# Performance work log

Measured on AMD Instinct MI355X. Metric: run time of the kernel, lower is better.

## Reference

```python
import jax, jax.numpy as jnp
import numpy as np

B = 2
C = 96
NH = 4
HD = C // NH
DEPTH = 2
LAT, LON = 181, 360
WH, WW = 6, 12
N = WH * WW
PT, PBm, PL, PR = 2, 3, 0, 0
H, W = LAT + PT + PBm, LON + PL + PR
SH, SW = WH // 2, WW // 2
NWH, NWW = H // WH, W // WW
NW = NWH * NWW
SCALE = HD ** -0.5

def _rel_index():
    ch, cw = np.meshgrid(np.arange(WH), np.arange(WW), indexing='ij')
    coords = np.stack([ch, cw]).reshape(2, -1)
    rel = (coords[:, :, None] - coords[:, None, :]).transpose(1, 2, 0).astype(np.int64)
    rel[:, :, 0] += WH - 1
    rel[:, :, 1] += WW - 1
    rel[:, :, 0] *= 2 * WW - 1
    return rel.sum(-1)  # (N, N)

REL_IDX = jnp.asarray(_rel_index())

def _shift_mask():
    img = np.zeros((H, W))
    cnt = 0
    for hs in (slice(0, -WH), slice(-WH, -SH), slice(-SH, None)):
        for ws in (slice(0, -WW), slice(-WW, -SW), slice(-SW, None)):
            img[hs, ws] = cnt
            cnt += 1
    mw = img.reshape(NWH, WH, NWW, WW).transpose(0, 2, 1, 3).reshape(NW, N)
    am = mw[:, None, :] - mw[:, :, None]
    return np.where(am != 0, -100.0, 0.0).astype(np.float32)

ATTN_MASK = jnp.asarray(_shift_mask())  # (NW, N, N)

def _ln(x, g, b):
    m = x.mean(-1, keepdims=True)
    v = x.var(-1, keepdims=True)
    return (x - m) * jax.lax.rsqrt(v + 1e-5) * g + b

def _win_part(x):
    b = x.shape[0]
    return x.reshape(b, NWH, WH, NWW, WW, C).transpose(0, 1, 3, 2, 4, 5).reshape(-1, N, C)

def _win_rev(xw, b):
    return xw.reshape(b, NWH, NWW, WH, WW, C).transpose(0, 1, 3, 2, 4, 5).reshape(b, H, W, C)

def _block(x, shift, g1, b1, qw, qb, pw, pb, rpb, g2, b2, f1w, f1b, f2w, f2b):
    b = x.shape[0]
    sc = x
    x = _ln(x, g1, b1)
    if shift:
        x = jnp.roll(x, (-SH, -SW), (1, 2))
    xw = _win_part(x)  # (b*NW, N, C)
    qkv = (xw @ qw.T + qb).reshape(-1, N, 3, NH, HD).transpose(2, 0, 3, 1, 4)
    q, k, v = qkv[0], qkv[1], qkv[2]  # each (b*NW, NH, N, HD)
    attn = (q * SCALE) @ k.transpose(0, 1, 3, 2)  # (b*NW, NH, N, N)
    bias = rpb[REL_IDX].transpose(2, 0, 1)  # (NH, N, N)
    attn = attn + bias[None]
    if shift:
        attn = (attn.reshape(b, NW, NH, N, N) + ATTN_MASK[None, :, None]).reshape(-1, NH, N, N)
    attn = jax.nn.softmax(attn, axis=-1)
    out = (attn @ v).transpose(0, 2, 1, 3).reshape(-1, N, C)
    out = out @ pw.T + pb
    x = _win_rev(out, b)
    if shift:
        x = jnp.roll(x, (SH, SW), (1, 2))
    x = sc + x
    h = _ln(x, g2, b2)
    h = jax.nn.gelu(h @ f1w.T + f1b) @ f2w.T + f2b
    return x + h

def _forward(x, g1, b1, qkv_w, qkv_b, proj_w, proj_b, rpb, g2, b2, fc1_w, fc1_b, fc2_w, fc2_b):
    x = jnp.pad(x, ((0, 0), (0, 0), (PT, PBm), (PL, PR)))  # ZeroPad2d
    x = x.transpose(0, 2, 3, 1)  # (B, H, W, C)
    for i in range(DEPTH):
        x = _block(x, i % 2 == 1, g1[i], b1[i], qkv_w[i], qkv_b[i], proj_w[i], proj_b[i],
                   rpb[i], g2[i], b2[i], fc1_w[i], fc1_b[i], fc2_w[i], fc2_b[i])
    x = x.transpose(0, 3, 1, 2)
    return x[:, :, PT:H - PBm, PL:W - PR]


def setup_inputs() -> dict:
    key = jax.random.key(0)
    ks = jax.random.split(key, 6)
    s = 0.02
    tbl = (2 * WH - 1) * (2 * WW - 1)
    return {
        'x': jax.random.normal(ks[0], (B, C, LAT, LON), jnp.float32),
        'g1': jnp.ones((DEPTH, C), jnp.float32),
        'b1': jnp.zeros((DEPTH, C), jnp.float32),
        'qkv_w': jax.random.normal(ks[1], (DEPTH, 3 * C, C), jnp.float32) * s,
        'qkv_b': jnp.zeros((DEPTH, 3 * C), jnp.float32),
        'proj_w': jax.random.normal(ks[2], (DEPTH, C, C), jnp.float32) * s,
        'proj_b': jnp.zeros((DEPTH, C), jnp.float32),
        'rpb': jax.random.normal(ks[3], (DEPTH, tbl, NH), jnp.float32) * s,
        'g2': jnp.ones((DEPTH, C), jnp.float32),
        'b2': jnp.zeros((DEPTH, C), jnp.float32),
        'fc1_w': jax.random.normal(ks[4], (DEPTH, 4 * C, C), jnp.float32) * s,
        'fc1_b': jnp.zeros((DEPTH, 4 * C), jnp.float32),
        'fc2_w': jax.random.normal(ks[5], (DEPTH, C, 4 * C), jnp.float32) * s,
        'fc2_b': jnp.zeros((DEPTH, C), jnp.float32),
    }


def reference(x, g1, b1, qkv_w, qkv_b, proj_w, proj_b, rpb, g2, b2, fc1_w, fc1_b, fc2_w, fc2_b):
    return _forward(x, g1, b1, qkv_w, qkv_b, proj_w, proj_b, rpb, g2, b2, fc1_w, fc1_b, fc2_w, fc2_b)
```

## Files before the change

kernel.cpp:

```cpp
#include <hip/hip_runtime.h>
#include <hip/hip_bf16.h>
#include <math.h>

#define BB    2
#define CC    96
#define NHD   4
#define HDIM  24
#define LAT_  181
#define LON_  360
#define PT_   2
#define HH    186
#define WWID  360
#define WH_   6
#define WW_   12
#define NTOK  72
#define SH_   3
#define SW_   6
#define NWH_  31
#define NWW_  30
#define NWIN  930
#define SCALE_ 0.20412414523193154f

typedef __attribute__((ext_vector_type(8))) short short8v;
typedef __attribute__((ext_vector_type(4))) float f32x4;

__device__ __forceinline__ unsigned short pk_bf16(float x) {
    __hip_bfloat16 h = __float2bfloat16(x);
    union { __hip_bfloat16 b; unsigned short u; } cv; cv.b = h; return cv.u;
}
__device__ __forceinline__ uint2 pk4(float a, float b, float c, float d) {
    __hip_bfloat162 lo = __float22bfloat162_rn(make_float2(a, b));
    __hip_bfloat162 hi = __float22bfloat162_rn(make_float2(c, d));
    union { __hip_bfloat162 b; unsigned u; } c0, c1; c0.b = lo; c1.b = hi;
    uint2 r; r.x = c0.u; r.y = c1.u; return r;
}

__global__ __launch_bounds__(256) void k_pad2(const float* __restrict__ in, float* __restrict__ X) {
    int bid = blockIdx.x;
    int ct = bid % 3; bid /= 3;
    int wt = bid % 12; bid /= 12;
    int h = bid % HH; int b = bid / HH;
    int lat = h - PT_;
    int tx = threadIdx.x & 31, ty = threadIdx.x >> 5;
    __shared__ float tile[32][33];
    if (lat >= 0 && lat < LAT_) {
        int w = wt * 32 + tx;
        #pragma unroll
        for (int i = 0; i < 4; ++i) {
            int c = ct * 32 + ty + 8 * i;
            float v = 0.f;
            if (w < WWID) v = in[((long)(b * CC + c)) * (LAT_ * LON_) + lat * LON_ + w];
            tile[ty + 8 * i][tx] = v;
        }
    } else {
        #pragma unroll
        for (int i = 0; i < 4; ++i) tile[ty + 8 * i][tx] = 0.f;
    }
    __syncthreads();
    #pragma unroll
    for (int i = 0; i < 4; ++i) {
        int w = wt * 32 + ty + 8 * i;
        if (w < WWID)
            X[(((long)(b * HH + h)) * WWID + w) * CC + ct * 32 + tx] = tile[tx][ty + 8 * i];
    }
}

__global__ __launch_bounds__(256) void k_crop2(const float* __restrict__ X, float* __restrict__ out) {
    int bid = blockIdx.x;
    int ct = bid % 3; bid /= 3;
    int wt = bid % 12; bid /= 12;
    int lat = bid % LAT_; int b = bid / LAT_;
    int h = lat + PT_;
    int tx = threadIdx.x & 31, ty = threadIdx.x >> 5;
    __shared__ float tile[32][33];
    #pragma unroll
    for (int i = 0; i < 4; ++i) {
        int w = wt * 32 + ty + 8 * i;
        if (w < WWID)
            tile[ty + 8 * i][tx] = X[(((long)(b * HH + h)) * WWID + w) * CC + ct * 32 + tx];
    }
    __syncthreads();
    {
        int w = wt * 32 + tx;
        if (w < WWID) {
            #pragma unroll
            for (int i = 0; i < 4; ++i) {
                int c = ct * 32 + ty + 8 * i;
                out[((long)(b * CC + c)) * (LAT_ * LON_) + lat * LON_ + w] = tile[tx][ty + 8 * i];
            }
        }
    }
}

__global__ void k_wprep(const float* __restrict__ f1w, const float* __restrict__ f2w,
                        const float* __restrict__ qkvw, const float* __restrict__ projw,
                        const float* __restrict__ rpb,
                        unsigned short* __restrict__ wbf, float* __restrict__ biasg) {
    int id = blockIdx.x * 256 + threadIdx.x;
    if (id < 73728) {
        int layer = id / 36864, rem = id % 36864;
        int ks = rem / 12288, r2 = rem % 12288;
        int nt = r2 / 512, r3 = r2 % 512;
        int lane = r3 / 8, e = r3 % 8;
        int o = nt * 16 + (lane & 15);
        int c = ks * 32 + 8 * (lane >> 4) + e;
        wbf[(long)layer * 36864 + rem] = pk_bf16(f1w[((long)layer * 384 + o) * 96 + c]);
    } else if (id < 147456) {
        int id2 = id - 73728;
        int layer = id2 / 36864, rem = id2 % 36864;
        int ks = rem / 3072, r2 = rem % 3072;
        int nt = r2 / 512, r3 = r2 % 512;
        int lane = r3 / 8, e = r3 % 8;
        int o = nt * 16 + (lane & 15);
        int c = ks * 32 + 8 * (lane >> 4) + e;
        wbf[73728 + (long)layer * 36864 + rem] = pk_bf16(f2w[((long)layer * 96 + o) * 384 + c]);
    } else if (id < 202752) {
        wbf[id] = pk_bf16(qkvw[id - 147456]);
    } else if (id < 221184) {
        wbf[id] = pk_bf16(projw[id - 202752]);
    } else {
        int id2 = id - 221184;
        int layer = id2 / 102400, r = id2 % 102400;
        int type = r / 25600; r %= 25600;
        int h = r / 6400; r %= 6400;
        int i = r / 80, j = r % 80;
        float v;
        if (i >= 72 || j >= 72) {
            v = -10000.f;
        } else {
            int thi = i / 12, twi = i % 12, thj = j / 12, twj = j % 12;
            int ridx = (thi - thj + 5) * 23 + (twi - twj + 11);
            v = rpb[(layer * 253 + ridx) * 4 + h];
            if (layer == 1) {
                int eh = type & 1, ew = type >> 1;
                int ri = (eh ? (thi < 3 ? 1 : 2) * 3 : 0) + (ew ? (twi < 6 ? 1 : 2) : 0);
                int rj = (eh ? (thj < 3 ? 1 : 2) * 3 : 0) + (ew ? (twj < 6 ? 1 : 2) : 0);
                if (ri != rj) v -= 100.f;
            }
        }
        biasg[id2] = v;
    }
}

template <int SHIFT>
__global__ __launch_bounds__(1024, 4) void k_attn(float* __restrict__ X,
        const float* __restrict__ gg, const float* __restrict__ bb,
        const unsigned short* __restrict__ wqkv, const float* __restrict__ qkvb,
        const unsigned short* __restrict__ wprj, const float* __restrict__ projb,
        const float* __restrict__ biasT) {
    __shared__ __align__(16) unsigned char smem[127232];
    unsigned short* As  = (unsigned short*)smem;
    unsigned short* psw0= (unsigned short*)smem;
    unsigned short* qs  = (unsigned short*)(smem + 53248);
    unsigned short* ks  = (unsigned short*)(smem + 68608);
    unsigned short* vt  = (unsigned short*)(smem + 83968);
    unsigned short* os  = (unsigned short*)(smem + 110592);

    int bid = blockIdx.x;
    int b = bid / NWIN, wi = bid % NWIN;
    int nwh = wi / NWW_, nww = wi % NWW_;
    int tid = threadIdx.x;
    int wv = tid >> 6, lane = tid & 63;
    int li = lane & 15, gq = lane >> 4;

    int type = SHIFT ? ((nwh == 30 ? 1 : 0) | (nww == 29 ? 2 : 0)) : 0;
    const float* bias_t = biasT + type * 25600;

    {
        unsigned* vz = (unsigned*)vt;
        for (int idx = tid; idx < 6656; idx += 1024) vz[idx] = 0u;
        unsigned* az = (unsigned*)(As + 72 * 104);
        for (int idx = tid; idx < 416; idx += 1024) az[idx] = 0u;
    }

    {
        int sub = lane >> 3, p = lane & 7;
        int t = wv * 8 + sub;
        if (t < 72) {
            int th = t / 12, tw = t % 12;
            int hr = nwh * WH_ + th, wr = nww * WW_ + tw;
            int ho = SHIFT ? (hr + SH_) % HH : hr;
            int wo = SHIFT ? (wr + SW_) % WWID : wr;
            const float* xr = X + (((long)b * HH + ho) * WWID + wo) * CC;
            float4 a  = *(const float4*)(xr + p * 4);
            float4 c4 = *(const float4*)(xr + p * 4 + 32);
            float4 e4 = *(const float4*)(xr + p * 4 + 64);
            float s  = a.x + a.y + a.z + a.w + c4.x + c4.y + c4.z + c4.w + e4.x + e4.y + e4.z + e4.w;
            float sq = a.x*a.x + a.y*a.y + a.z*a.z + a.w*a.w + c4.x*c4.x + c4.y*c4.y + c4.z*c4.z + c4.w*c4.w
                     + e4.x*e4.x + e4.y*e4.y + e4.z*e4.z + e4.w*e4.w;
            #pragma unroll
            for (int off = 1; off < 8; off <<= 1) {
                s  += __shfl_xor(s, off);
                sq += __shfl_xor(sq, off);
            }
            float mean = s * (1.f / CC);
            float var = sq * (1.f / CC) - mean * mean;
            float rs = rsqrtf(var + 1e-5f);
            float4 g0 = *(const float4*)(gg + p * 4);
            float4 g1v = *(const float4*)(gg + p * 4 + 32);
            float4 g2v = *(const float4*)(gg + p * 4 + 64);
            float4 t0 = *(const float4*)(bb + p * 4);
            float4 t1 = *(const float4*)(bb + p * 4 + 32);
            float4 t2 = *(const float4*)(bb + p * 4 + 64);
            *(uint2*)(As + t * 104 + p * 4) =
                pk4((a.x - mean) * rs * g0.x + t0.x, (a.y - mean) * rs * g0.y + t0.y,
                    (a.z - mean) * rs * g0.z + t0.z, (a.w - mean) * rs * g0.w + t0.w);
            *(uint2*)(As + t * 104 + p * 4 + 32) =
                pk4((c4.x - mean) * rs * g1v.x + t1.x, (c4.y - mean) * rs * g1v.y + t1.y,
                    (c4.z - mean) * rs * g1v.z + t1.z, (c4.w - mean) * rs * g1v.w + t1.w);
            *(uint2*)(As + t * 104 + p * 4 + 64) =
                pk4((e4.x - mean) * rs * g2v.x + t2.x, (e4.y - mean) * rs * g2v.y + t2.y,
                    (e4.z - mean) * rs * g2v.z + t2.z, (e4.w - mean) * rs * g2v.w + t2.w);
        }
    }
    __syncthreads();

    for (int mt = wv; mt < 18; mt += 16) {
        short8v aw[3];
        #pragma unroll
        for (int ksi = 0; ksi < 3; ++ksi)
            aw[ksi] = *(const short8v*)(wqkv + (mt * 16 + li) * 96 + ksi * 32 + 8 * gq);
        float bias4[4];
        #pragma unroll
        for (int r = 0; r < 4; ++r) bias4[r] = qkvb[mt * 16 + 4 * gq + r];
        f32x4 acc[5];
        #pragma unroll
        for (int nt = 0; nt < 5; ++nt) acc[nt] = (f32x4){0.f, 0.f, 0.f, 0.f};
        #pragma unroll
        for (int nt = 0; nt < 5; ++nt)
            #pragma unroll
            for (int ksi = 0; ksi < 3; ++ksi) {
                short8v by = *(const short8v*)(As + (nt * 16 + li) * 104 + ksi * 32 + 8 * gq);
                acc[nt] = __builtin_amdgcn_mfma_f32_16x16x32_bf16(aw[ksi], by, acc[nt], 0, 0, 0);
            }
        int which = mt / 6, mtl = mt % 6;
        int oo0 = mtl * 16 + 4 * gq;
        int h = oo0 / 24, d0 = oo0 % 24;
        #pragma unroll
        for (int nt = 0; nt < 5; ++nt) {
            int token = nt * 16 + li;
            if (which == 2) {
                #pragma unroll
                for (int r = 0; r < 4; ++r)
                    vt[(h * 32 + d0 + r) * 104 + token] = pk_bf16(acc[nt][r] + bias4[r]);
            } else {
                float v0 = acc[nt][0] + bias4[0], v1 = acc[nt][1] + bias4[1];
                float v2 = acc[nt][2] + bias4[2], v3 = acc[nt][3] + bias4[3];
                if (which == 0) { v0 *= SCALE_; v1 *= SCALE_; v2 *= SCALE_; v3 *= SCALE_; }
                unsigned short* dst = (which == 0 ? qs : ks) + (h * 80 + token) * 24 + d0;
                *(uint2*)dst = pk4(v0, v1, v2, v3);
            }
        }
    }
    __syncthreads();

    for (int u = wv; u < 20; u += 16) {
        int h = u / 5, nt = u % 5;
        unsigned short* psw = psw0 + (size_t)wv * (16 * 104);
        *(uint2*)(psw + li * 104 + 80 + 4 * gq) = (uint2){0u, 0u};
        short8v bq = {0,0,0,0,0,0,0,0};
        if (gq < 3) bq = *(const short8v*)(qs + (h * 80 + nt * 16 + li) * 24 + 8 * gq);
        const float* brow = bias_t + (h * 80 + nt * 16 + li) * 80;
        float p[20];
        float sum = 0.f;
        #pragma unroll
        for (int mt = 0; mt < 5; ++mt) {
            short8v ak = {0,0,0,0,0,0,0,0};
            if (gq < 3) ak = *(const short8v*)(ks + (h * 80 + mt * 16 + li) * 24 + 8 * gq);
            f32x4 ct = __builtin_amdgcn_mfma_f32_16x16x32_bf16(ak, bq, (f32x4){0.f,0.f,0.f,0.f}, 0, 0, 0);
            float4 bv = *(const float4*)(brow + mt * 16 + 4 * gq);
            p[mt*4+0] = __expf(ct[0] + bv.x);
            p[mt*4+1] = __expf(ct[1] + bv.y);
            p[mt*4+2] = __expf(ct[2] + bv.z);
            p[mt*4+3] = __expf(ct[3] + bv.w);
            sum += p[mt*4+0] + p[mt*4+1] + p[mt*4+2] + p[mt*4+3];
        }
        sum += __shfl_xor(sum, 16);
        sum += __shfl_xor(sum, 32);
        float inv = sum > 0.f ? 1.f / sum : 0.f;
        #pragma unroll
        for (int mt = 0; mt < 5; ++mt)
            *(uint2*)(psw + li * 104 + mt * 16 + 4 * gq) =
                pk4(p[mt*4+0] * inv, p[mt*4+1] * inv, p[mt*4+2] * inv, p[mt*4+3] * inv);
        #pragma unroll
        for (int nt2 = 0; nt2 < 2; ++nt2) {
            f32x4 acc = (f32x4){0.f, 0.f, 0.f, 0.f};
            #pragma unroll
            for (int ksi = 0; ksi < 3; ++ksi) {
                short8v ap = *(const short8v*)(psw + li * 104 + ksi * 32 + 8 * gq);
                short8v bv = *(const short8v*)(vt + (h * 32 + nt2 * 16 + li) * 104 + ksi * 32 + 8 * gq);
                acc = __builtin_amdgcn_mfma_f32_16x16x32_bf16(ap, bv, acc, 0, 0, 0);
            }
            int d = nt2 * 16 + li;
            if (d < 24) {
                #pragma unroll
                for (int r = 0; r < 4; ++r)
                    os[(nt * 16 + 4 * gq + r) * 104 + h * 24 + d] = pk_bf16(acc[r]);
            }
        }
    }
    __syncthreads();

    for (int u = wv; u < 30; u += 16) {
        int mt = u / 6, nt = u % 6;
        f32x4 acc = (f32x4){0.f, 0.f, 0.f, 0.f};
        #pragma unroll
        for (int ksi = 0; ksi < 3; ++ksi) {
            short8v ao = *(const short8v*)(os + (mt * 16 + li) * 104 + ksi * 32 + 8 * gq);
            short8v bw = *(const short8v*)(wprj + (nt * 16 + li) * 96 + ksi * 32 + 8 * gq);
            acc = __builtin_amdgcn_mfma_f32_16x16x32_bf16(ao, bw, acc, 0, 0, 0);
        }
        int o = nt * 16 + li;
        float bo = projb[o];
        #pragma unroll
        for (int r = 0; r < 4; ++r) {
            int token = mt * 16 + 4 * gq + r;
            if (token < 72) {
                int th = token / 12, tw = token % 12;
                int hr = nwh * WH_ + th, wr = nww * WW_ + tw;
                int ho = SHIFT ? (hr + SH_) % HH : hr;
                int wo = SHIFT ? (wr + SW_) % WWID : wr;
                X[(((long)b * HH + ho) * WWID + wo) * CC + o] += acc[r] + bo;
            }
        }
    }
}

__global__ __launch_bounds__(256, 4) void k_mlp_mfma(float* __restrict__ X,
        const float* __restrict__ g, const float* __restrict__ bta,
        const unsigned short* __restrict__ w1f, const float* __restrict__ b1v,
        const unsigned short* __restrict__ w2f, const float* __restrict__ b2v) {
    __shared__ __align__(16) unsigned short As[32 * 120];
    __shared__ __align__(16) unsigned short Hs[32 * 392];
    long tok0 = (long)blockIdx.x * 32;
    int tid = threadIdx.x;

    {
        int t = tid >> 3, p = tid & 7;
        const float* xr = X + (tok0 + t) * CC;
        float4 a = *(const float4*)(xr + p * 4);
        float4 b = *(const float4*)(xr + p * 4 + 32);
        float4 c4 = *(const float4*)(xr + p * 4 + 64);
        float s  = a.x + a.y + a.z + a.w + b.x + b.y + b.z + b.w + c4.x + c4.y + c4.z + c4.w;
        float sq = a.x*a.x + a.y*a.y + a.z*a.z + a.w*a.w + b.x*b.x + b.y*b.y + b.z*b.z + b.w*b.w
                 + c4.x*c4.x + c4.y*c4.y + c4.z*c4.z + c4.w*c4.w;
        #pragma unroll
        for (int off = 1; off < 8; off <<= 1) {
            s  += __shfl_xor(s, off);
            sq += __shfl_xor(sq, off);
        }
        float mean = s * (1.f / CC);
        float var = sq * (1.f / CC) - mean * mean;
        float rs = rsqrtf(var + 1e-5f);
        float4 g0 = *(const float4*)(g + p * 4);
        float4 g1 = *(const float4*)(g + p * 4 + 32);
        float4 g2 = *(const float4*)(g + p * 4 + 64);
        float4 t0 = *(const float4*)(bta + p * 4);
        float4 t1 = *(const float4*)(bta + p * 4 + 32);
        float4 t2 = *(const float4*)(bta + p * 4 + 64);
        unsigned short* arow = As + t * 120;
        *(uint2*)(arow + p * 4) =
            pk4((a.x - mean) * rs * g0.x + t0.x, (a.y - mean) * rs * g0.y + t0.y,
                (a.z - mean) * rs * g0.z + t0.z, (a.w - mean) * rs * g0.w + t0.w);
        *(uint2*)(arow + p * 4 + 32) =
            pk4((b.x - mean) * rs * g1.x + t1.x, (b.y - mean) * rs * g1.y + t1.y,
                (b.z - mean) * rs * g1.z + t1.z, (b.w - mean) * rs * g1.w + t1.w);
        *(uint2*)(arow + p * 4 + 64) =
            pk4((c4.x - mean) * rs * g2.x + t2.x, (c4.y - mean) * rs * g2.y + t2.y,
                (c4.z - mean) * rs * g2.z + t2.z, (c4.w - mean) * rs * g2.w + t2.w);
    }
    __syncthreads();

    int w = tid >> 6, lane = tid & 63;
    int wm = w & 1;
    int row = wm * 16 + (lane & 15);
    int kbase = 8 * (lane >> 4);

    {
        int wnh = w >> 1;
        short8v afr[3];
        #pragma unroll
        for (int ks = 0; ks < 3; ++ks)
            afr[ks] = *(const short8v*)(As + row * 120 + ks * 32 + kbase);
        f32x4 acc[12];
        #pragma unroll
        for (int j = 0; j < 12; ++j) acc[j] = (f32x4){0.f, 0.f, 0.f, 0.f};
        const short8v* wb = (const short8v*)w1f;
        #pragma unroll
        for (int j = 0; j < 12; ++j) {
            int nt = wnh * 12 + j;
            #pragma unroll
            for (int ks = 0; ks < 3; ++ks) {
                short8v bfr = wb[(ks * 24 + nt) * 64 + lane];
                acc[j] = __builtin_amdgcn_mfma_f32_16x16x32_bf16(afr[ks], bfr, acc[j], 0, 0, 0);
            }
        }
        #pragma unroll
        for (int j = 0; j < 12; ++j) {
            int n = (wnh * 12 + j) * 16 + (lane & 15);
            float bb = b1v[n];
            #pragma unroll
            for (int r = 0; r < 4; ++r) {
                float s = acc[j][r] + bb;
                float z = s + 0.044715f * s * s * s;
                float gl = s / (1.f + __expf(-1.5957691216057308f * z));
                Hs[(wm * 16 + 4 * (lane >> 4) + r) * 392 + n] = pk_bf16(gl);
            }
        }
    }
    __syncthreads();

    {
        int wnt0 = (w >> 1) * 3;
        f32x4 acc2[3];
        #pragma unroll
        for (int j = 0; j < 3; ++j) acc2[j] = (f32x4){0.f, 0.f, 0.f, 0.f};
        const short8v* wb2 = (const short8v*)w2f;
        #pragma unroll
        for (int ks = 0; ks < 12; ++ks) {
            short8v a2 = *(const short8v*)(Hs + row * 392 + ks * 32 + kbase);
            #pragma unroll
            for (int j = 0; j < 3; ++j) {
                short8v bfr = wb2[(ks * 6 + wnt0 + j) * 64 + lane];
                acc2[j] = __builtin_amdgcn_mfma_f32_16x16x32_bf16(a2, bfr, acc2[j], 0, 0, 0);
            }
        }
        #pragma unroll
        for (int j = 0; j < 3; ++j) {
            int n = (wnt0 + j) * 16 + (lane & 15);
            float bb = b2v[n];
            #pragma unroll
            for (int r = 0; r < 4; ++r) {
                long tok = tok0 + wm * 16 + 4 * (lane >> 4) + r;
                X[tok * CC + n] += acc2[j][r] + bb;
            }
        }
    }
}

extern "C" void kernel_launch(void* const* d_in, const int* in_sizes, int n_in,
                              void* d_out, int out_size, void* d_ws, size_t ws_size,
                              hipStream_t stream) {
    const float* x     = (const float*)d_in[0];
    const float* g1    = (const float*)d_in[1];
    const float* b1    = (const float*)d_in[2];
    const float* qkvw  = (const float*)d_in[3];
    const float* qkvb  = (const float*)d_in[4];
    const float* projw = (const float*)d_in[5];
    const float* projb = (const float*)d_in[6];
    const float* rpb   = (const float*)d_in[7];
    const float* g2    = (const float*)d_in[8];
    const float* b2    = (const float*)d_in[9];
    const float* f1w   = (const float*)d_in[10];
    const float* f1b   = (const float*)d_in[11];
    const float* f2w   = (const float*)d_in[12];
    const float* f2b   = (const float*)d_in[13];

    float* X = (float*)d_ws;
    unsigned short* wbf = (unsigned short*)(X + (long)BB * HH * WWID * CC);
    float* biasg = (float*)(wbf + 221184);

    const int ntok = BB * HH * WWID;

    k_pad2<<<BB * HH * 12 * 3, 256, 0, stream>>>(x, X);
    k_wprep<<<1664, 256, 0, stream>>>(f1w, f2w, qkvw, projw, rpb, wbf, biasg);

    for (int i = 0; i < 2; ++i) {
        const unsigned short* wqkv_bf = wbf + 147456 + (long)i * 27648;
        const unsigned short* wprj_bf = wbf + 202752 + (long)i * 9216;
        if (i == 0) {
            k_attn<0><<<BB * NWIN, 1024, 0, stream>>>(X, g1, b1,
                wqkv_bf, qkvb, wprj_bf, projb, biasg);
        } else {
            k_attn<1><<<BB * NWIN, 1024, 0, stream>>>(X, g1 + CC, b1 + CC,
                wqkv_bf, qkvb + 3 * CC, wprj_bf, projb + CC, biasg + 102400);
        }
        k_mlp_mfma<<<ntok / 32, 256, 0, stream>>>(X,
            g2 + i * CC, b2 + i * CC,
            wbf + (long)i * 36864, f1b + i * 4 * CC,
            wbf + 73728 + (long)i * 36864, f2b + i * CC);
    }

    k_crop2<<<BB * LAT_ * 12 * 3, 256, 0, stream>>>(X, (float*)d_out);
}
```

Baseline: 326.7 us.

## Fuse MLP block into windowed attention kernel per window

The second LayerNorm and the two-layer MLP now run inside the attention kernel. The post-projection residual is kept in shared memory (Xn) for the window's 72 tokens, so the separate MLP kernel launch and a full read-modify-write pass over X in global memory go away. The cost is that the MLP now runs in 1024-thread blocks with heavy shared memory use, which limits occupancy. It also wastes work on padded rows, since 80 rows are computed for 72 tokens.

```diff
diff --git a/kernel.cpp b/kernel.cpp
--- a/kernel.cpp
+++ b/kernel.cpp
@@ -147,7 +147,10 @@
         const float* __restrict__ gg, const float* __restrict__ bb,
         const unsigned short* __restrict__ wqkv, const float* __restrict__ qkvb,
         const unsigned short* __restrict__ wprj, const float* __restrict__ projb,
-        const float* __restrict__ biasT) {
+        const float* __restrict__ biasT,
+        const float* __restrict__ g2, const float* __restrict__ b2,
+        const unsigned short* __restrict__ w1f, const float* __restrict__ b1v,
+        const unsigned short* __restrict__ w2f, const float* __restrict__ b2v) {
     __shared__ __align__(16) unsigned char smem[127232];
     unsigned short* As  = (unsigned short*)smem;
     unsigned short* psw0= (unsigned short*)smem;
@@ -155,6 +158,9 @@
     unsigned short* ks  = (unsigned short*)(smem + 68608);
     unsigned short* vt  = (unsigned short*)(smem + 83968);
     unsigned short* os  = (unsigned short*)(smem + 110592);
+    float* Xn           = (float*)smem;
+    unsigned short* A2s = (unsigned short*)(smem + 33280);
+    unsigned short* Hs  = (unsigned short*)(smem + 53248);
 
     int bid = blockIdx.x;
     int b = bid / NWIN, wi = bid % NWIN;
@@ -172,7 +178,6 @@
         unsigned* az = (unsigned*)(As + 72 * 104);
         for (int idx = tid; idx < 416; idx += 1024) az[idx] = 0u;
     }
-
     {
         int sub = lane >> 3, p = lane & 7;
         int t = wv * 8 + sub;
@@ -320,119 +325,102 @@
                 int hr = nwh * WH_ + th, wr = nww * WW_ + tw;
                 int ho = SHIFT ? (hr + SH_) % HH : hr;
                 int wo = SHIFT ? (wr + SW_) % WWID : wr;
-                X[(((long)b * HH + ho) * WWID + wo) * CC + o] += acc[r] + bo;
-            }
-        }
-    }
-}
-
-__global__ __launch_bounds__(256, 4) void k_mlp_mfma(float* __restrict__ X,
-        const float* __restrict__ g, const float* __restrict__ bta,
-        const unsigned short* __restrict__ w1f, const float* __restrict__ b1v,
-        const unsigned short* __restrict__ w2f, const float* __restrict__ b2v) {
-    __shared__ __align__(16) unsigned short As[32 * 120];
-    __shared__ __align__(16) unsigned short Hs[32 * 392];
-    long tok0 = (long)blockIdx.x * 32;
-    int tid = threadIdx.x;
+                float xo = X[(((long)b * HH + ho) * WWID + wo) * CC + o];
+                Xn[token * 104 + o] = xo + acc[r] + bo;
+            }
+        }
+    }
+    __syncthreads();
 
     {
-        int t = tid >> 3, p = tid & 7;
-        const float* xr = X + (tok0 + t) * CC;
-        float4 a = *(const float4*)(xr + p * 4);
-        float4 b = *(const float4*)(xr + p * 4 + 32);
-        float4 c4 = *(const float4*)(xr + p * 4 + 64);
-        float s  = a.x + a.y + a.z + a.w + b.x + b.y + b.z + b.w + c4.x + c4.y + c4.z + c4.w;
-        float sq = a.x*a.x + a.y*a.y + a.z*a.z + a.w*a.w + b.x*b.x + b.y*b.y + b.z*b.z + b.w*b.w
-                 + c4.x*c4.x + c4.y*c4.y + c4.z*c4.z + c4.w*c4.w;
-        #pragma unroll
-        for (int off = 1; off < 8; off <<= 1) {
-            s  += __shfl_xor(s, off);
-            sq += __shfl_xor(sq, off);
-        }
-        float mean = s * (1.f / CC);
-        float var = sq * (1.f / CC) - mean * mean;
-        float rs = rsqrtf(var + 1e-5f);
-        float4 g0 = *(const float4*)(g + p * 4);
-        float4 g1 = *(const float4*)(g + p * 4 + 32);
-        float4 g2 = *(const float4*)(g + p * 4 + 64);
-        float4 t0 = *(const float4*)(bta + p * 4);
-        float4 t1 = *(const float4*)(bta + p * 4 + 32);
-        float4 t2 = *(const float4*)(bta + p * 4 + 64);
-        unsigned short* arow = As + t * 120;
-        *(uint2*)(arow + p * 4) =
-            pk4((a.x - mean) * rs * g0.x + t0.x, (a.y - mean) * rs * g0.y + t0.y,
-                (a.z - mean) * rs * g0.z + t0.z, (a.w - mean) * rs * g0.w + t0.w);
-        *(uint2*)(arow + p * 4 + 32) =
-            pk4((b.x - mean) * rs * g1.x + t1.x, (b.y - mean) * rs * g1.y + t1.y,
-                (b.z - mean) * rs * g1.z + t1.z, (b.w - mean) * rs * g1.w + t1.w);
-        *(uint2*)(arow + p * 4 + 64) =
-            pk4((c4.x - mean) * rs * g2.x + t2.x, (c4.y - mean) * rs * g2.y + t2.y,
-                (c4.z - mean) * rs * g2.z + t2.z, (c4.w - mean) * rs * g2.w + t2.w);
-    }
-    __syncthreads();
-
-    int w = tid >> 6, lane = tid & 63;
-    int wm = w & 1;
-    int row = wm * 16 + (lane & 15);
-    int kbase = 8 * (lane >> 4);
-
+        unsigned* az = (unsigned*)(A2s + 72 * 104);
+        for (int idx = tid; idx < 416; idx += 1024) az[idx] = 0u;
+    }
     {
-        int wnh = w >> 1;
+        int sub = lane >> 3, p = lane & 7;
+        int t = wv * 8 + sub;
+        if (t < 72) {
+            const float* xr = Xn + t * 104;
+            float4 a  = *(const float4*)(xr + p * 4);
+            float4 c4 = *(const float4*)(xr + p * 4 + 32);
+            float4 e4 = *(const float4*)(xr + p * 4 + 64);
+            float s  = a.x + a.y + a.z + a.w + c4.x + c4.y + c4.z + c4.w + e4.x + e4.y + e4.z + e4.w;
+            float sq = a.x*a.x + a.y*a.y + a.z*a.z + a.w*a.w + c4.x*c4.x + c4.y*c4.y + c4.z*c4.z + c4.w*c4.w
+                     + e4.x*e4.x + e4.y*e4.y + e4.z*e4.z + e4.w*e4.w;
+            #pragma unroll
+            for (int off = 1; off < 8; off <<= 1) {
+                s  += __shfl_xor(s, off);
+                sq += __shfl_xor(sq, off);
+            }
+            float mean = s * (1.f / CC);
+            float var = sq * (1.f / CC) - mean * mean;
+            float rs = rsqrtf(var + 1e-5f);
+            float4 g0 = *(const float4*)(g2 + p * 4);
+            float4 g1v = *(const float4*)(g2 + p * 4 + 32);
+            float4 g2v = *(const float4*)(g2 + p * 4 + 64);
+            float4 t0 = *(const float4*)(b2 + p * 4);
+            float4 t1 = *(const float4*)(b2 + p * 4 + 32);
+            float4 t2 = *(const float4*)(b2 + p * 4 + 64);
+            *(uint2*)(A2s + t * 104 + p * 4) =
+                pk4((a.x - mean) * rs * g0.x + t0.x, (a.y - mean) * rs * g0.y + t0.y,
+                    (a.z - mean) * rs * g0.z + t0.z, (a.w - mean) * rs * g0.w + t0.w);
+            *(uint2*)(A2s + t * 104 + p * 4 + 32) =
+                pk4((c4.x - mean) * rs * g1v.x + t1.x, (c4.y - mean) * rs * g1v.y + t1.y,
+                    (c4.z - mean) * rs * g1v.z + t1.z, (c4.w - mean) * rs * g1v.w + t1.w);
+            *(uint2*)(A2s + t * 104 + p * 4 + 64) =
+                pk4((e4.x - mean) * rs * g2v.x + t2.x, (e4.y - mean) * rs * g2v.y + t2.y,
+                    (e4.z - mean) * rs * g2v.z + t2.z, (e4.w - mean) * rs * g2v.w + t2.w);
+        }
+    }
+    __syncthreads();
+
+    for (int u = wv; u < 120; u += 16) {
+        int mt = u / 24, nt = u % 24;
         short8v afr[3];
         #pragma unroll
-        for (int ks = 0; ks < 3; ++ks)
-            afr[ks] = *(const short8v*)(As + row * 120 + ks * 32 + kbase);
-        f32x4 acc[12];
-        #pragma unroll
-        for (int j = 0; j < 12; ++j) acc[j] = (f32x4){0.f, 0.f, 0.f, 0.f};
+        for (int ksi = 0; ksi < 3; ++ksi)
+            afr[ksi] = *(const short8v*)(A2s + (mt * 16 + li) * 104 + ksi * 32 + 8 * gq);
+        f32x4 acc = (f32x4){0.f, 0.f, 0.f, 0.f};
         const short8v* wb = (const short8v*)w1f;
         #pragma unroll
-        for (int j = 0; j < 12; ++j) {
-            int nt = wnh * 12 + j;
-            #pragma unroll
-            for (int ks = 0; ks < 3; ++ks) {
-                short8v bfr = wb[(ks * 24 + nt) * 64 + lane];
-                acc[j] = __builtin_amdgcn_mfma_f32_16x16x32_bf16(afr[ks], bfr, acc[j], 0, 0, 0);
-            }
-        }
-        #pragma unroll
-        for (int j = 0; j < 12; ++j) {
-            int n = (wnh * 12 + j) * 16 + (lane & 15);
-            float bb = b1v[n];
-            #pragma unroll
-            for (int r = 0; r < 4; ++r) {
-                float s = acc[j][r] + bb;
-                float z = s + 0.044715f * s * s * s;
-                float gl = s / (1.f + __expf(-1.5957691216057308f * z));
-                Hs[(wm * 16 + 4 * (lane >> 4) + r) * 392 + n] = pk_bf16(gl);
-            }
-        }
-    }
-    __syncthreads();
-
-    {
-        int wnt0 = (w >> 1) * 3;
-        f32x4 acc2[3];
-        #pragma unroll
-        for (int j = 0; j < 3; ++j) acc2[j] = (f32x4){0.f, 0.f, 0.f, 0.f};
+        for (int ksi = 0; ksi < 3; ++ksi) {
+            short8v bfr = wb[(ksi * 24 + nt) * 64 + lane];
+            acc = __builtin_amdgcn_mfma_f32_16x16x32_bf16(afr[ksi], bfr, acc, 0, 0, 0);
+        }
+        int n = nt * 16 + li;
+        float bb1 = b1v[n];
+        #pragma unroll
+        for (int r = 0; r < 4; ++r) {
+            float s = acc[r] + bb1;
+            float z = s + 0.044715f * s * s * s;
+            float gl = s / (1.f + __expf(-1.5957691216057308f * z));
+            Hs[(mt * 16 + 4 * gq + r) * 392 + n] = pk_bf16(gl);
+        }
+    }
+    __syncthreads();
+
+    for (int u = wv; u < 30; u += 16) {
+        int mt = u / 6, nt = u % 6;
+        f32x4 acc = (f32x4){0.f, 0.f, 0.f, 0.f};
         const short8v* wb2 = (const short8v*)w2f;
         #pragma unroll
-        for (int ks = 0; ks < 12; ++ks) {
-            short8v a2 = *(const short8v*)(Hs + row * 392 + ks * 32 + kbase);
-            #pragma unroll
-            for (int j = 0; j < 3; ++j) {
-                short8v bfr = wb2[(ks * 6 + wnt0 + j) * 64 + lane];
-                acc2[j] = __builtin_amdgcn_mfma_f32_16x16x32_bf16(a2, bfr, acc2[j], 0, 0, 0);
-            }
-        }
-        #pragma unroll
-        for (int j = 0; j < 3; ++j) {
-            int n = (wnt0 + j) * 16 + (lane & 15);
-            float bb = b2v[n];
-            #pragma unroll
-            for (int r = 0; r < 4; ++r) {
-                long tok = tok0 + wm * 16 + 4 * (lane >> 4) + r;
-                X[tok * CC + n] += acc2[j][r] + bb;
+        for (int ksi = 0; ksi < 12; ++ksi) {
+            short8v a2 = *(const short8v*)(Hs + (mt * 16 + li) * 392 + ksi * 32 + 8 * gq);
+            short8v bfr = wb2[(ksi * 6 + nt) * 64 + lane];
+            acc = __builtin_amdgcn_mfma_f32_16x16x32_bf16(a2, bfr, acc, 0, 0, 0);
+        }
+        int n = nt * 16 + li;
+        float bb2 = b2v[n];
+        #pragma unroll
+        for (int r = 0; r < 4; ++r) {
+            int token = mt * 16 + 4 * gq + r;
+            if (token < 72) {
+                int th = token / 12, tw = token % 12;
+                int hr = nwh * WH_ + th, wr = nww * WW_ + tw;
+                int ho = SHIFT ? (hr + SH_) % HH : hr;
+                int wo = SHIFT ? (wr + SW_) % WWID : wr;
+                X[(((long)b * HH + ho) * WWID + wo) * CC + n] =
+                    Xn[token * 104 + n] + acc[r] + bb2;
             }
         }
     }
@@ -460,25 +448,23 @@
     unsigned short* wbf = (unsigned short*)(X + (long)BB * HH * WWID * CC);
     float* biasg = (float*)(wbf + 221184);
 
-    const int ntok = BB * HH * WWID;
-
     k_pad2<<<BB * HH * 12 * 3, 256, 0, stream>>>(x, X);
     k_wprep<<<1664, 256, 0, stream>>>(f1w, f2w, qkvw, projw, rpb, wbf, biasg);
 
     for (int i = 0; i < 2; ++i) {
         const unsigned short* wqkv_bf = wbf + 147456 + (long)i * 27648;
         const unsigned short* wprj_bf = wbf + 202752 + (long)i * 9216;
+        const unsigned short* w1f = wbf + (long)i * 36864;
+        const unsigned short* w2f = wbf + 73728 + (long)i * 36864;
         if (i == 0) {
             k_attn<0><<<BB * NWIN, 1024, 0, stream>>>(X, g1, b1,
-                wqkv_bf, qkvb, wprj_bf, projb, biasg);
+                wqkv_bf, qkvb, wprj_bf, projb, biasg,
+                g2, b2, w1f, f1b, w2f, f2b);
         } else {
             k_attn<1><<<BB * NWIN, 1024, 0, stream>>>(X, g1 + CC, b1 + CC,
-                wqkv_bf, qkvb + 3 * CC, wprj_bf, projb + CC, biasg + 102400);
-        }
-        k_mlp_mfma<<<ntok / 32, 256, 0, stream>>>(X,
-            g2 + i * CC, b2 + i * CC,
-            wbf + (long)i * 36864, f1b + i * 4 * CC,
-            wbf + 73728 + (long)i * 36864, f2b + i * CC);
+                wqkv_bf, qkvb + 3 * CC, wprj_bf, projb + CC, biasg + 102400,
+                g2 + CC, b2 + CC, w1f, f1b + 4 * CC, w2f, f2b + CC);
+        }
     }
 
     k_crop2<<<BB * LAT_ * 12 * 3, 256, 0, stream>>>(X, (float*)d_out);
```

Result: slower. 373.7 us (+14.4%).

## Keep softmax probabilities in registers via lane shuffles and shrink shared memory

Applied to the files above, without the earlier changes.

The normalized attention probabilities are no longer staged through a per-wave shared-memory scratch buffer. They are redistributed across lanes with shuffles directly into the MFMA A-operand layout. This removes the psw region, so the LDS layout is repacked to about 74KB and the launch bounds ask for more resident blocks, aiming for higher occupancy and fewer LDS round trips. The cost is many extra shuffle instructions and possible register pressure under the tighter launch bound.

```diff
diff --git a/kernel.cpp b/kernel.cpp
--- a/kernel.cpp
+++ b/kernel.cpp
@@ -143,18 +143,17 @@
 }
 
 template <int SHIFT>
-__global__ __launch_bounds__(1024, 4) void k_attn(float* __restrict__ X,
+__global__ __launch_bounds__(1024, 8) void k_attn(float* __restrict__ X,
         const float* __restrict__ gg, const float* __restrict__ bb,
         const unsigned short* __restrict__ wqkv, const float* __restrict__ qkvb,
         const unsigned short* __restrict__ wprj, const float* __restrict__ projb,
         const float* __restrict__ biasT) {
-    __shared__ __align__(16) unsigned char smem[127232];
+    __shared__ __align__(16) unsigned char smem[73984];
     unsigned short* As  = (unsigned short*)smem;
-    unsigned short* psw0= (unsigned short*)smem;
-    unsigned short* qs  = (unsigned short*)(smem + 53248);
-    unsigned short* ks  = (unsigned short*)(smem + 68608);
-    unsigned short* vt  = (unsigned short*)(smem + 83968);
-    unsigned short* os  = (unsigned short*)(smem + 110592);
+    unsigned short* os  = (unsigned short*)smem;
+    unsigned short* qs  = (unsigned short*)(smem + 16640);
+    unsigned short* ks  = (unsigned short*)(smem + 32000);
+    unsigned short* vt  = (unsigned short*)(smem + 47360);
 
     int bid = blockIdx.x;
     int b = bid / NWIN, wi = bid % NWIN;
@@ -256,8 +255,6 @@
 
     for (int u = wv; u < 20; u += 16) {
         int h = u / 5, nt = u % 5;
-        unsigned short* psw = psw0 + (size_t)wv * (16 * 104);
-        *(uint2*)(psw + li * 104 + 80 + 4 * gq) = (uint2){0u, 0u};
         short8v bq = {0,0,0,0,0,0,0,0};
         if (gq < 3) bq = *(const short8v*)(qs + (h * 80 + nt * 16 + li) * 24 + 8 * gq);
         const float* brow = bias_t + (h * 80 + nt * 16 + li) * 80;
@@ -279,17 +276,32 @@
         sum += __shfl_xor(sum, 32);
         float inv = sum > 0.f ? 1.f / sum : 0.f;
         #pragma unroll
-        for (int mt = 0; mt < 5; ++mt)
-            *(uint2*)(psw + li * 104 + mt * 16 + 4 * gq) =
-                pk4(p[mt*4+0] * inv, p[mt*4+1] * inv, p[mt*4+2] * inv, p[mt*4+3] * inv);
+        for (int k2 = 0; k2 < 20; ++k2) p[k2] *= inv;
+
+        short8v ap[3];
+        #pragma unroll
+        for (int ksi = 0; ksi < 3; ++ksi) {
+            float pv[8];
+            #pragma unroll
+            for (int e = 0; e < 8; ++e) {
+                int srcl = li + 16 * (2 * (gq & 1) + (e >> 2));
+                float s0 = __shfl(p[8 * ksi + (e & 3)], srcl);
+                float s1 = (ksi < 2) ? __shfl(p[8 * ksi + 4 + (e & 3)], srcl) : 0.f;
+                pv[e] = (gq >= 2) ? s1 : s0;
+            }
+            uint2 lo = pk4(pv[0], pv[1], pv[2], pv[3]);
+            uint2 hi = pk4(pv[4], pv[5], pv[6], pv[7]);
+            union { uint4 u; short8v s; } cvt;
+            cvt.u = make_uint4(lo.x, lo.y, hi.x, hi.y);
+            ap[ksi] = cvt.s;
+        }
         #pragma unroll
         for (int nt2 = 0; nt2 < 2; ++nt2) {
             f32x4 acc = (f32x4){0.f, 0.f, 0.f, 0.f};
             #pragma unroll
             for (int ksi = 0; ksi < 3; ++ksi) {
-                short8v ap = *(const short8v*)(psw + li * 104 + ksi * 32 + 8 * gq);
-                short8v bv = *(const short8v*)(vt + (h * 32 + nt2 * 16 + li) * 104 + ksi * 32 + 8 * gq);
-                acc = __builtin_amdgcn_mfma_f32_16x16x32_bf16(ap, bv, acc, 0, 0, 0);
+                short8v bv2 = *(const short8v*)(vt + (h * 32 + nt2 * 16 + li) * 104 + ksi * 32 + 8 * gq);
+                acc = __builtin_amdgcn_mfma_f32_16x16x32_bf16(ap[ksi], bv2, acc, 0, 0, 0);
             }
             int d = nt2 * 16 + li;
             if (d < 24) {
```

Measured after the change: 306.0 us. -6.3%, faster.
